# Kernel tuning notes

Measured on AMD Instinct MI355X. Metric: run time of the kernel, lower is better.

The kernel has to match this reference:

```python
import jax, jax.numpy as jnp
import numpy as np

N = 50000      # nodes
E0 = 400000    # random edges (before self loops)
F_IN = 64      # in_channels == out_channels (required by the view in forward)
H = 2          # heads
C = 64         # per-head out_channels
B, T = 1, 8
NEG_SLOPE = 0.2


def setup_inputs() -> dict:
    key = jax.random.key(0)
    ks = jax.random.split(key, 7)
    self_loops = jnp.arange(N, dtype=jnp.int32)  # GATConv add_self_loops=True
    src = jnp.concatenate([jax.random.randint(ks[0], (E0,), 0, N, dtype=jnp.int32), self_loops])
    dst = jnp.concatenate([jax.random.randint(ks[1], (E0,), 0, N, dtype=jnp.int32), self_loops])
    h = jax.random.normal(ks[2], (B, N, T, F_IN), dtype=jnp.float32)
    glorot = float(np.sqrt(2.0 / (F_IN + H * C)))
    W = jax.random.normal(ks[3], (F_IN, H, C), dtype=jnp.float32) * glorot
    att_src = jax.random.normal(ks[4], (H, C), dtype=jnp.float32) * 0.1
    att_dst = jax.random.normal(ks[5], (H, C), dtype=jnp.float32) * 0.1
    bias = jax.random.normal(ks[6], (C,), dtype=jnp.float32) * 0.1
    return {"h": h, "src": src, "dst": dst, "W": W,
            "att_src": att_src, "att_dst": att_dst, "bias": bias}


def _gat_step(xt, src, dst, W, att_src, att_dst, bias, n_nodes):
    # xt: [N, F_in] node features for one timestep
    xl = jnp.einsum('nf,fhc->nhc', xt, W)               # [N, H, C]
    a_s = jnp.einsum('nhc,hc->nh', xl, att_src)          # source score per node
    a_d = jnp.einsum('nhc,hc->nh', xl, att_dst)          # dest score per node
    e = jax.nn.leaky_relu(a_s[src] + a_d[dst], NEG_SLOPE)  # [E, H]
    # segment softmax over incoming edges of each destination node
    emax = jax.ops.segment_max(e, dst, num_segments=n_nodes)
    ex = jnp.exp(e - emax[dst])
    denom = jax.ops.segment_sum(ex, dst, num_segments=n_nodes)
    alpha = ex / denom[dst]                              # [E, H]
    msg = alpha[:, :, None] * xl[src]                    # [E, H, C]
    out = jax.ops.segment_sum(msg, dst, num_segments=n_nodes)  # [N, H, C]
    out = out.mean(axis=1) + bias                        # concat=False: head mean
    return jax.nn.elu(out)


def reference(h, src, dst, W, att_src, att_dst, bias):
    Bn, Nn, Tn, Fin = h.shape
    # [B, N, T, F] -> [B*T, N, F] (matches h.transpose(1,2).view(-1, N, F))
    x = jnp.transpose(h, (0, 2, 1, 3)).reshape(Bn * Tn, Nn, Fin)

    def step(carry, xt):
        return carry, _gat_step(xt, src, dst, W, att_src, att_dst, bias, Nn)

    _, outs = jax.lax.scan(step, None, x)                # [B*T, N, C]
    out = outs.reshape(Bn, Tn, Nn, -1)
    return jnp.transpose(out, (0, 2, 1, 3))              # [B, N, T, C]
```

## Files before the change

### kernel.cpp

```cpp
#include <hip/hip_runtime.h>
#include <hip/hip_bf16.h>
#include <math.h>

#define T_STEPS 8
#define F_IN 64
#define HC 128
#define C_OUT 64
#define NEG_SLOPE 0.2f

typedef _Float16 half8 __attribute__((ext_vector_type(8)));
typedef _Float16 half2v __attribute__((ext_vector_type(2)));
typedef float f32x4 __attribute__((ext_vector_type(4)));

static __device__ __forceinline__ float dot2(half2v a, half2v b, float c) {
    return __builtin_amdgcn_fdot2(a, b, c, false);
}

__global__ void k_zero_i32(int* p, int n) {
    int i = blockIdx.x * blockDim.x + threadIdx.x;
    if (i < n) p[i] = 0;
}

__global__ void k_count(const int* __restrict__ dst, int* __restrict__ cnt, int E) {
    int e = blockIdx.x * blockDim.x + threadIdx.x;
    if (e < E) atomicAdd(&cnt[dst[e]], 1);
}

__global__ void k_scan1(int* data, int* bsum, int n) {
    __shared__ int tmp[256];
    int tid = threadIdx.x;
    int i = blockIdx.x * 256 + tid;
    int v = (i < n) ? data[i] : 0;
    tmp[tid] = v; __syncthreads();
    for (int off = 1; off < 256; off <<= 1) {
        int x = (tid >= off) ? tmp[tid - off] : 0;
        __syncthreads();
        tmp[tid] += x;
        __syncthreads();
    }
    if (i < n) data[i] = tmp[tid] - v;
    if (tid == 255) bsum[blockIdx.x] = tmp[255];
}

__global__ void k_scan2(int* bsum, int nb) {
    __shared__ int tmp[256];
    int tid = threadIdx.x;
    int v = (tid < nb) ? bsum[tid] : 0;
    tmp[tid] = v; __syncthreads();
    for (int off = 1; off < 256; off <<= 1) {
        int x = (tid >= off) ? tmp[tid - off] : 0;
        __syncthreads();
        tmp[tid] += x;
        __syncthreads();
    }
    if (tid < nb) bsum[tid] = tmp[tid] - v;
}

__global__ void k_scan3(int* data, const int* __restrict__ bsum, int* cursor, int n, int total) {
    int i = blockIdx.x * 256 + threadIdx.x;
    if (i < n) {
        int v = data[i] + bsum[i >> 8];
        data[i] = v;
        cursor[i] = v;
    }
    if (i == 0) data[n] = total;
}

__global__ void k_fill(const int* __restrict__ src, const int* __restrict__ dst,
                       int* __restrict__ cursor, int* __restrict__ csr_src, int E) {
    int e = blockIdx.x * blockDim.x + threadIdx.x;
    if (e < E) {
        int d = dst[e];
        int pos = atomicAdd(&cursor[d], 1);
        csr_src[pos] = src[e];
    }
}

__global__ void k_prep(const float* __restrict__ W, const float* __restrict__ att_src,
                       const float* __restrict__ att_dst,
                       _Float16* __restrict__ Wt, _Float16* __restrict__ WQt) {
    int b = blockIdx.x;
    int tid = threadIdx.x;
    if (b == 0) {
        int q = tid & 3, f = tid >> 2;
        const float* att = (q & 2) ? att_dst : att_src;
        int hh = q & 1;
        float s = 0.f;
        #pragma unroll 8
        for (int c = 0; c < 64; c++) s += W[f * HC + hh * 64 + c] * att[hh * 64 + c];
        WQt[q * 64 + f] = (_Float16)s;
    } else {
        int i = (b - 1) * 256 + tid;
        int ei = i >> 6, k = i & 63;
        Wt[i] = (_Float16)W[k * HC + (ei & 1) * 64 + (ei >> 1)];
    }
}

__global__ __launch_bounds__(256) void k_gemm(
    const float* __restrict__ h, const _Float16* __restrict__ Wt,
    const _Float16* __restrict__ WQt,
    _Float16* __restrict__ xlh, float* __restrict__ a_s, float* __restrict__ a_d,
    int N)
{
    __shared__ _Float16 smem[64 * 136];
    _Float16* sA   = smem;
    _Float16* sOut = smem;

    int tid = threadIdx.x;
    int t = blockIdx.y;
    int node0 = blockIdx.x * 64;
    int w = tid >> 6;
    int lane = tid & 63;
    int cl = lane & 15;
    int lg = lane >> 4;

    {
        int row = tid >> 2;
        int k0 = (tid & 3) * 16;
        int n = node0 + row;
        int nc = n < N ? n : N - 1;
        const float* hp = h + ((size_t)nc * T_STEPS + t) * F_IN + k0;
        f32x4 x0 = __builtin_nontemporal_load((const f32x4*)(hp));
        f32x4 x1 = __builtin_nontemporal_load((const f32x4*)(hp + 4));
        f32x4 x2 = __builtin_nontemporal_load((const f32x4*)(hp + 8));
        f32x4 x3 = __builtin_nontemporal_load((const f32x4*)(hp + 12));
        half8 p0, p1;
        p0[0] = (_Float16)x0[0]; p0[1] = (_Float16)x0[1];
        p0[2] = (_Float16)x0[2]; p0[3] = (_Float16)x0[3];
        p0[4] = (_Float16)x1[0]; p0[5] = (_Float16)x1[1];
        p0[6] = (_Float16)x1[2]; p0[7] = (_Float16)x1[3];
        p1[0] = (_Float16)x2[0]; p1[1] = (_Float16)x2[1];
        p1[2] = (_Float16)x2[2]; p1[3] = (_Float16)x2[3];
        p1[4] = (_Float16)x3[0]; p1[5] = (_Float16)x3[1];
        p1[6] = (_Float16)x3[2]; p1[7] = (_Float16)x3[3];
        *(half8*)&sA[row * 72 + k0]     = p0;
        *(half8*)&sA[row * 72 + k0 + 8] = p1;
    }
    __syncthreads();

    half8 af[4][2];
    #pragma unroll
    for (int rt = 0; rt < 4; rt++)
        #pragma unroll
        for (int ks = 0; ks < 2; ks++)
            af[rt][ks] = *(half8*)&sA[(rt * 16 + cl) * 72 + ks * 32 + lg * 8];

    half8 bf[2][2];
    #pragma unroll
    for (int ct = 0; ct < 2; ct++)
        #pragma unroll
        for (int ks = 0; ks < 2; ks++)
            bf[ct][ks] = *(const half8*)&Wt[(size_t)(w * 32 + ct * 16 + cl) * 64 + ks * 32 + lg * 8];

    half8 bq[2];
    #pragma unroll
    for (int ks = 0; ks < 2; ks++) {
        half8 b = {};
        if (cl < 4) b = *(const half8*)&WQt[cl * 64 + ks * 32 + lg * 8];
        bq[ks] = b;
    }

    __syncthreads();

    #pragma unroll
    for (int rt = 0; rt < 4; rt++)
        #pragma unroll
        for (int ct = 0; ct < 2; ct++) {
            f32x4 c = {0.f, 0.f, 0.f, 0.f};
            c = __builtin_amdgcn_mfma_f32_16x16x32_f16(af[rt][0], bf[ct][0], c, 0, 0, 0);
            c = __builtin_amdgcn_mfma_f32_16x16x32_f16(af[rt][1], bf[ct][1], c, 0, 0, 0);
            int slot = w * 32 + ct * 16 + cl;
            #pragma unroll
            for (int reg = 0; reg < 4; reg++)
                sOut[(rt * 16 + lg * 4 + reg) * 136 + slot] = (_Float16)c[reg];
        }

    f32x4 sacc = {0.f, 0.f, 0.f, 0.f};
    sacc = __builtin_amdgcn_mfma_f32_16x16x32_f16(af[w][0], bq[0], sacc, 0, 0, 0);
    sacc = __builtin_amdgcn_mfma_f32_16x16x32_f16(af[w][1], bq[1], sacc, 0, 0, 0);

    float* ast = a_s + (size_t)t * N * 2;
    float* adt = a_d + (size_t)t * N * 2;
    if (cl < 4) {
        float* basep = (cl & 2) ? adt : ast;
        #pragma unroll
        for (int reg = 0; reg < 4; reg++) {
            int n = node0 + w * 16 + lg * 4 + reg;
            if (n < N) basep[(size_t)n * 2 + (cl & 1)] = sacc[reg];
        }
    }

    __syncthreads();

    _Float16* xlt = xlh + (size_t)t * N * HC;
    #pragma unroll
    for (int it = 0; it < 4; it++) {
        int idx = it * 256 + tid;
        int row = idx >> 4;
        int seg = idx & 15;
        int n = node0 + row;
        if (n < N)
            *(half8*)&xlt[(size_t)n * HC + seg * 8] = *(half8*)&sOut[row * 136 + seg * 8];
    }
}

__global__ __launch_bounds__(256) void k_edge(
    const int* __restrict__ csr_row, const int* __restrict__ csr_src,
    const float* __restrict__ a_s, const float* __restrict__ a_d,
    const _Float16* __restrict__ xlh, const float* __restrict__ bias,
    float* __restrict__ out, int N)
{
    __shared__ int2 edata[16][16];

    int tid  = threadIdx.x;
    int lane = tid & 63;
    int wid  = tid >> 6;
    int grp  = lane >> 4;
    int gl   = lane & 15;
    int t = blockIdx.y;
    const _Float16* xlt = xlh + (size_t)t * N * HC;
    const char* xb = (const char*)xlt;
    int l4 = lane * 4;
    const float* ast = a_s + (size_t)t * N * 2;
    const float* adt = a_d + (size_t)t * N * 2;

    int nodeBlock0 = blockIdx.x * 16;
    int node = nodeBlock0 + wid * 4 + grp;
    bool nvalid = node < N;

    int beg = 0, end = 0;
    if (nvalid) { beg = csr_row[node]; end = csr_row[node + 1]; }
    int deg = end - beg;

    float bs = bias[lane];

    if (__ballot(deg > 16) == 0ull) {
        float2 adv = make_float2(0.f, 0.f);
        if (nvalid) adv = *(const float2*)&adt[(size_t)node * 2];

        int e = beg + gl;
        bool ev = nvalid && (e < end);
        int s = ev ? csr_src[e] : 0;
        float e0 = -1e30f, e1 = -1e30f;
        if (ev) {
            float2 asv = *(const float2*)&ast[(size_t)s * 2];
            e0 = asv.x + adv.x;
            e1 = asv.y + adv.y;
            e0 = e0 > 0.f ? e0 : NEG_SLOPE * e0;
            e1 = e1 > 0.f ? e1 : NEG_SLOPE * e1;
        }
        float m0 = e0, m1 = e1;
        #pragma unroll
        for (int off = 8; off >= 1; off >>= 1) {
            m0 = fmaxf(m0, __shfl_xor(m0, off));
            m1 = fmaxf(m1, __shfl_xor(m1, off));
        }
        float x0 = ev ? __expf(e0 - m0) : 0.f;
        float x1 = ev ? __expf(e1 - m1) : 0.f;
        float d0 = x0, d1 = x1;
        #pragma unroll
        for (int off = 8; off >= 1; off >>= 1) {
            d0 += __shfl_xor(d0, off);
            d1 += __shfl_xor(d1, off);
        }
        float w0 = x0 * (0.5f / d0);
        float w1 = x1 * (0.5f / d1);

        union { uint u; _Float16 hh[2]; } cw;
        cw.hh[0] = ev ? (_Float16)w0 : (_Float16)0.f;
        cw.hh[1] = ev ? (_Float16)w1 : (_Float16)0.f;
        edata[wid * 4 + grp][gl] = make_int2(ev ? (s << 8) : 0, (int)cw.u);

        #pragma unroll
        for (int k = 0; k < 4; k++) {
            int nk = nodeBlock0 + wid * 4 + k;
            if (nk >= N) continue;
            int dk = __shfl(deg, k * 16);
            int dkr = (dk + 7) & ~7;
            float a0 = 0.f, a1 = 0.f;
            const int2* row = edata[wid * 4 + k];
            for (int j = 0; j < dkr; j += 8) {
                int4 p  = *(const int4*)&row[j];
                int4 q  = *(const int4*)&row[j + 2];
                int4 r2 = *(const int4*)&row[j + 4];
                int4 s2 = *(const int4*)&row[j + 6];
                half2v v0 = *(const half2v*)(xb + p.x  + l4);
                half2v v1 = *(const half2v*)(xb + p.z  + l4);
                half2v v2 = *(const half2v*)(xb + q.x  + l4);
                half2v v3 = *(const half2v*)(xb + q.z  + l4);
                half2v v4 = *(const half2v*)(xb + r2.x + l4);
                half2v v5 = *(const half2v*)(xb + r2.z + l4);
                half2v v6 = *(const half2v*)(xb + s2.x + l4);
                half2v v7 = *(const half2v*)(xb + s2.z + l4);
                union { int i; half2v h; } c0, c1, c2, c3, c4, c5, c6, c7;
                c0.i = p.y;  c1.i = p.w;
                c2.i = q.y;  c3.i = q.w;
                c4.i = r2.y; c5.i = r2.w;
                c6.i = s2.y; c7.i = s2.w;
                a0 = dot2(v0, c0.h, a0);
                a1 = dot2(v1, c1.h, a1);
                a0 = dot2(v2, c2.h, a0);
                a1 = dot2(v3, c3.h, a1);
                a0 = dot2(v4, c4.h, a0);
                a1 = dot2(v5, c5.h, a1);
                a0 = dot2(v6, c6.h, a0);
                a1 = dot2(v7, c7.h, a1);
            }
            float acc = a0 + a1 + bs;
            float o = acc > 0.f ? acc : expm1f(acc);
            __builtin_nontemporal_store(o, &out[((size_t)nk * T_STEPS + t) * C_OUT + lane]);
        }
    } else {
        #pragma unroll
        for (int k = 0; k < 4; k++) {
            int nk = nodeBlock0 + wid * 4 + k;
            if (nk >= N) continue;
            int bk = __shfl(beg, k * 16);
            int ek = __shfl(end, k * 16);
            float2 adv = *(const float2*)&adt[(size_t)nk * 2];

            float m0 = -1e30f, m1 = -1e30f;
            for (int e = bk + lane; e < ek; e += 64) {
                int s = csr_src[e];
                float2 asv = *(const float2*)&ast[(size_t)s * 2];
                float e0 = asv.x + adv.x, e1 = asv.y + adv.y;
                e0 = e0 > 0.f ? e0 : NEG_SLOPE * e0;
                e1 = e1 > 0.f ? e1 : NEG_SLOPE * e1;
                m0 = fmaxf(m0, e0); m1 = fmaxf(m1, e1);
            }
            #pragma unroll
            for (int off = 32; off >= 1; off >>= 1) {
                m0 = fmaxf(m0, __shfl_xor(m0, off));
                m1 = fmaxf(m1, __shfl_xor(m1, off));
            }
            float d0 = 0.f, d1 = 0.f;
            for (int e = bk + lane; e < ek; e += 64) {
                int s = csr_src[e];
                float2 asv = *(const float2*)&ast[(size_t)s * 2];
                float e0 = asv.x + adv.x, e1 = asv.y + adv.y;
                e0 = e0 > 0.f ? e0 : NEG_SLOPE * e0;
                e1 = e1 > 0.f ? e1 : NEG_SLOPE * e1;
                d0 += __expf(e0 - m0); d1 += __expf(e1 - m1);
            }
            #pragma unroll
            for (int off = 32; off >= 1; off >>= 1) {
                d0 += __shfl_xor(d0, off);
                d1 += __shfl_xor(d1, off);
            }
            float r0 = 0.5f / d0, r1 = 0.5f / d1;

            float a0 = 0.f, a1 = 0.f;
            for (int base = bk; base < ek; base += 64) {
                int e = base + lane;
                int cnt = min(64, ek - base);
                int soff = 0;
                union { uint u; _Float16 hh[2]; } cw;
                cw.u = 0u;
                if (e < ek) {
                    int s = csr_src[e];
                    soff = s << 8;
                    float2 asv = *(const float2*)&ast[(size_t)s * 2];
                    float e0 = asv.x + adv.x, e1 = asv.y + adv.y;
                    e0 = e0 > 0.f ? e0 : NEG_SLOPE * e0;
                    e1 = e1 > 0.f ? e1 : NEG_SLOPE * e1;
                    cw.hh[0] = (_Float16)(__expf(e0 - m0) * r0);
                    cw.hh[1] = (_Float16)(__expf(e1 - m1) * r1);
                }
                int wv = (int)cw.u;
                for (int j = 0; j < cnt; j++) {
                    int sj = __shfl(soff, j);
                    int wj = __shfl(wv, j);
                    union { int i; half2v h; } c; c.i = wj;
                    half2v v = *(const half2v*)(xb + sj + l4);
                    a0 = dot2(v, c.h, a0);
                }
            }
            float acc = a0 + a1 + bs;
            float o = acc > 0.f ? acc : expm1f(acc);
            __builtin_nontemporal_store(o, &out[((size_t)nk * T_STEPS + t) * C_OUT + lane]);
        }
    }
}

extern "C" void kernel_launch(void* const* d_in, const int* in_sizes, int n_in,
                              void* d_out, int out_size, void* d_ws, size_t ws_size,
                              hipStream_t stream)
{
    const float* h       = (const float*)d_in[0];
    const int*   src     = (const int*)d_in[1];
    const int*   dst     = (const int*)d_in[2];
    const float* W       = (const float*)d_in[3];
    const float* att_src = (const float*)d_in[4];
    const float* att_dst = (const float*)d_in[5];
    const float* bias    = (const float*)d_in[6];
    float* out = (float*)d_out;

    int N = in_sizes[0] / (T_STEPS * F_IN);
    int E = in_sizes[1];

    char* wsb = (char*)d_ws;
    size_t off = 0;
    auto alloc = [&](size_t bytes) -> char* {
        off = (off + 255) & ~(size_t)255;
        char* p = wsb + off;
        off += bytes;
        return p;
    };

    int* csr_row = (int*)alloc((size_t)(N + 1) * sizeof(int));
    int* cursor  = (int*)alloc((size_t)N * sizeof(int));
    int* bsum    = (int*)alloc(1024 * sizeof(int));
    int* csr_src = (int*)alloc((size_t)E * sizeof(int));
    float* a_s   = (float*)alloc((size_t)T_STEPS * N * 2 * sizeof(float));
    float* a_d   = (float*)alloc((size_t)T_STEPS * N * 2 * sizeof(float));
    _Float16* Wt  = (_Float16*)alloc((size_t)HC * 64 * sizeof(_Float16));
    _Float16* WQt = (_Float16*)alloc(4 * 64 * sizeof(_Float16));
    _Float16* xlh = (_Float16*)alloc((size_t)T_STEPS * N * HC * sizeof(_Float16));

    int nb = (N + 255) / 256;
    k_zero_i32<<<(N + 1 + 255) / 256, 256, 0, stream>>>(csr_row, N + 1);
    k_count<<<(E + 255) / 256, 256, 0, stream>>>(dst, csr_row, E);
    k_scan1<<<nb, 256, 0, stream>>>(csr_row, bsum, N);
    k_scan2<<<1, 256, 0, stream>>>(bsum, nb);
    k_scan3<<<nb, 256, 0, stream>>>(csr_row, bsum, cursor, N, E);
    k_fill<<<(E + 255) / 256, 256, 0, stream>>>(src, dst, cursor, csr_src, E);

    k_prep<<<33, 256, 0, stream>>>(W, att_src, att_dst, Wt, WQt);
    dim3 gg((N + 63) / 64, T_STEPS);
    k_gemm<<<gg, 256, 0, stream>>>(h, Wt, WQt, xlh, a_s, a_d, N);
    dim3 ge((N + 15) / 16, T_STEPS);
    k_edge<<<ge, 256, 0, stream>>>(csr_row, csr_src, a_s, a_d, xlh, bias, out, N);
}
```

Measured before the change: 439.8 us.

## Process four nodes per wave concurrently with 16-byte gathers in GAT edge kernel

The fast path now has each 16-lane group handle its own destination node. Each lane gathers a half8 (16 bytes) covering four output channels, instead of the whole wave looping over four nodes with 4-byte gathers per lane. The degree threshold for the fast path rises from 16 to 32, with two edges per lane staged in a wider shared array. Outputs are written as float4 nontemporal stores. This cuts loop iterations and memory instructions per edge, but the wave loop now runs to the largest degree among its four nodes, and each thread keeps more accumulators.

After: 418.5 us. 1.05x faster.

```diff
diff --git a/kernel.cpp b/kernel.cpp
--- a/kernel.cpp
+++ b/kernel.cpp
@@ -210,7 +210,7 @@
     const _Float16* __restrict__ xlh, const float* __restrict__ bias,
     float* __restrict__ out, int N)
 {
-    __shared__ int2 edata[16][16];
+    __shared__ int2 edata[16][34];
 
     int tid  = threadIdx.x;
     int lane = tid & 63;
@@ -220,7 +220,6 @@
     int t = blockIdx.y;
     const _Float16* xlt = xlh + (size_t)t * N * HC;
     const char* xb = (const char*)xlt;
-    int l4 = lane * 4;
     const float* ast = a_s + (size_t)t * N * 2;
     const float* adt = a_d + (size_t)t * N * 2;
 
@@ -232,85 +231,102 @@
     if (nvalid) { beg = csr_row[node]; end = csr_row[node + 1]; }
     int deg = end - beg;
 
-    float bs = bias[lane];
-
-    if (__ballot(deg > 16) == 0ull) {
+    if (__ballot(deg > 32) == 0ull) {
         float2 adv = make_float2(0.f, 0.f);
         if (nvalid) adv = *(const float2*)&adt[(size_t)node * 2];
 
-        int e = beg + gl;
-        bool ev = nvalid && (e < end);
-        int s = ev ? csr_src[e] : 0;
-        float e0 = -1e30f, e1 = -1e30f;
-        if (ev) {
-            float2 asv = *(const float2*)&ast[(size_t)s * 2];
-            e0 = asv.x + adv.x;
-            e1 = asv.y + adv.y;
-            e0 = e0 > 0.f ? e0 : NEG_SLOPE * e0;
-            e1 = e1 > 0.f ? e1 : NEG_SLOPE * e1;
-        }
-        float m0 = e0, m1 = e1;
+        int ea = beg + gl, eb = beg + gl + 16;
+        bool eva = nvalid && (ea < end);
+        bool evb = nvalid && (eb < end);
+        int sa = eva ? csr_src[ea] : 0;
+        int sb = evb ? csr_src[eb] : 0;
+        float ea0 = -1e30f, ea1 = -1e30f, eb0 = -1e30f, eb1 = -1e30f;
+        if (eva) {
+            float2 v = *(const float2*)&ast[(size_t)sa * 2];
+            ea0 = v.x + adv.x; ea1 = v.y + adv.y;
+            ea0 = ea0 > 0.f ? ea0 : NEG_SLOPE * ea0;
+            ea1 = ea1 > 0.f ? ea1 : NEG_SLOPE * ea1;
+        }
+        if (evb) {
+            float2 v = *(const float2*)&ast[(size_t)sb * 2];
+            eb0 = v.x + adv.x; eb1 = v.y + adv.y;
+            eb0 = eb0 > 0.f ? eb0 : NEG_SLOPE * eb0;
+            eb1 = eb1 > 0.f ? eb1 : NEG_SLOPE * eb1;
+        }
+        float m0 = fmaxf(ea0, eb0), m1 = fmaxf(ea1, eb1);
         #pragma unroll
         for (int off = 8; off >= 1; off >>= 1) {
             m0 = fmaxf(m0, __shfl_xor(m0, off));
             m1 = fmaxf(m1, __shfl_xor(m1, off));
         }
-        float x0 = ev ? __expf(e0 - m0) : 0.f;
-        float x1 = ev ? __expf(e1 - m1) : 0.f;
-        float d0 = x0, d1 = x1;
+        float xa0 = eva ? __expf(ea0 - m0) : 0.f;
+        float xa1 = eva ? __expf(ea1 - m1) : 0.f;
+        float xb0 = evb ? __expf(eb0 - m0) : 0.f;
+        float xb1 = evb ? __expf(eb1 - m1) : 0.f;
+        float d0 = xa0 + xb0, d1 = xa1 + xb1;
         #pragma unroll
         for (int off = 8; off >= 1; off >>= 1) {
             d0 += __shfl_xor(d0, off);
             d1 += __shfl_xor(d1, off);
         }
-        float w0 = x0 * (0.5f / d0);
-        float w1 = x1 * (0.5f / d1);
-
-        union { uint u; _Float16 hh[2]; } cw;
-        cw.hh[0] = ev ? (_Float16)w0 : (_Float16)0.f;
-        cw.hh[1] = ev ? (_Float16)w1 : (_Float16)0.f;
-        edata[wid * 4 + grp][gl] = make_int2(ev ? (s << 8) : 0, (int)cw.u);
-
-        #pragma unroll
-        for (int k = 0; k < 4; k++) {
-            int nk = nodeBlock0 + wid * 4 + k;
-            if (nk >= N) continue;
-            int dk = __shfl(deg, k * 16);
-            int dkr = (dk + 7) & ~7;
-            float a0 = 0.f, a1 = 0.f;
-            const int2* row = edata[wid * 4 + k];
-            for (int j = 0; j < dkr; j += 8) {
-                int4 p  = *(const int4*)&row[j];
-                int4 q  = *(const int4*)&row[j + 2];
-                int4 r2 = *(const int4*)&row[j + 4];
-                int4 s2 = *(const int4*)&row[j + 6];
-                half2v v0 = *(const half2v*)(xb + p.x  + l4);
-                half2v v1 = *(const half2v*)(xb + p.z  + l4);
-                half2v v2 = *(const half2v*)(xb + q.x  + l4);
-                half2v v3 = *(const half2v*)(xb + q.z  + l4);
-                half2v v4 = *(const half2v*)(xb + r2.x + l4);
-                half2v v5 = *(const half2v*)(xb + r2.z + l4);
-                half2v v6 = *(const half2v*)(xb + s2.x + l4);
-                half2v v7 = *(const half2v*)(xb + s2.z + l4);
-                union { int i; half2v h; } c0, c1, c2, c3, c4, c5, c6, c7;
-                c0.i = p.y;  c1.i = p.w;
-                c2.i = q.y;  c3.i = q.w;
-                c4.i = r2.y; c5.i = r2.w;
-                c6.i = s2.y; c7.i = s2.w;
-                a0 = dot2(v0, c0.h, a0);
-                a1 = dot2(v1, c1.h, a1);
-                a0 = dot2(v2, c2.h, a0);
-                a1 = dot2(v3, c3.h, a1);
-                a0 = dot2(v4, c4.h, a0);
-                a1 = dot2(v5, c5.h, a1);
-                a0 = dot2(v6, c6.h, a0);
-                a1 = dot2(v7, c7.h, a1);
-            }
-            float acc = a0 + a1 + bs;
-            float o = acc > 0.f ? acc : expm1f(acc);
-            __builtin_nontemporal_store(o, &out[((size_t)nk * T_STEPS + t) * C_OUT + lane]);
+        float r0 = 0.5f / d0, r1 = 0.5f / d1;
+
+        union { uint u; _Float16 hh[2]; } cwa, cwb;
+        cwa.hh[0] = (_Float16)(xa0 * r0); cwa.hh[1] = (_Float16)(xa1 * r1);
+        cwb.hh[0] = (_Float16)(xb0 * r0); cwb.hh[1] = (_Float16)(xb1 * r1);
+        int myrow = wid * 4 + grp;
+        edata[myrow][gl]      = make_int2(eva ? (sa << 8) : 0, (int)cwa.u);
+        edata[myrow][gl + 16] = make_int2(evb ? (sb << 8) : 0, (int)cwb.u);
+
+        int wmax = deg;
+        wmax = max(wmax, __shfl_xor(wmax, 16));
+        wmax = max(wmax, __shfl_xor(wmax, 32));
+        int dkr = (wmax + 3) & ~3;
+
+        const int2* row = edata[myrow];
+        int sb16 = gl * 16;
+        float ac0 = 0.f, ac1 = 0.f, ac2 = 0.f, ac3 = 0.f;
+        union h8u { half8 v; half2v h[4]; };
+        for (int j = 0; j < dkr; j += 4) {
+            int4 p = *(const int4*)&row[j];
+            int4 q = *(const int4*)&row[j + 2];
+            h8u v0, v1, v2, v3;
+            v0.v = *(const half8*)(xb + p.x + sb16);
+            v1.v = *(const half8*)(xb + p.z + sb16);
+            v2.v = *(const half8*)(xb + q.x + sb16);
+            v3.v = *(const half8*)(xb + q.z + sb16);
+            union { int i; half2v h; } w0, w1, w2, w3;
+            w0.i = p.y; w1.i = p.w; w2.i = q.y; w3.i = q.w;
+            ac0 = dot2(v0.h[0], w0.h, ac0);
+            ac1 = dot2(v0.h[1], w0.h, ac1);
+            ac2 = dot2(v0.h[2], w0.h, ac2);
+            ac3 = dot2(v0.h[3], w0.h, ac3);
+            ac0 = dot2(v1.h[0], w1.h, ac0);
+            ac1 = dot2(v1.h[1], w1.h, ac1);
+            ac2 = dot2(v1.h[2], w1.h, ac2);
+            ac3 = dot2(v1.h[3], w1.h, ac3);
+            ac0 = dot2(v2.h[0], w2.h, ac0);
+            ac1 = dot2(v2.h[1], w2.h, ac1);
+            ac2 = dot2(v2.h[2], w2.h, ac2);
+            ac3 = dot2(v2.h[3], w2.h, ac3);
+            ac0 = dot2(v3.h[0], w3.h, ac0);
+            ac1 = dot2(v3.h[1], w3.h, ac1);
+            ac2 = dot2(v3.h[2], w3.h, ac2);
+            ac3 = dot2(v3.h[3], w3.h, ac3);
+        }
+        if (nvalid) {
+            float4 bv = *(const float4*)&bias[gl * 4];
+            float c0 = ac0 + bv.x, c1 = ac1 + bv.y, c2 = ac2 + bv.z, c3 = ac3 + bv.w;
+            f32x4 o;
+            o[0] = c0 > 0.f ? c0 : expm1f(c0);
+            o[1] = c1 > 0.f ? c1 : expm1f(c1);
+            o[2] = c2 > 0.f ? c2 : expm1f(c2);
+            o[3] = c3 > 0.f ? c3 : expm1f(c3);
+            __builtin_nontemporal_store(o,
+                (f32x4*)&out[((size_t)node * T_STEPS + t) * C_OUT + gl * 4]);
         }
     } else {
+        float bs = bias[lane];
         #pragma unroll
         for (int k = 0; k < 4; k++) {
             int nk = nodeBlock0 + wid * 4 + k;
@@ -371,7 +387,7 @@
                     int sj = __shfl(soff, j);
                     int wj = __shfl(wv, j);
                     union { int i; half2v h; } c; c.i = wj;
-                    half2v v = *(const half2v*)(xb + sj + l4);
+                    half2v v = *(const half2v*)(xb + sj + lane * 4);
                     a0 = dot2(v, c.h, a0);
                 }
             }
```
